# Kernel tuning notes

Measured on AMD Instinct MI355X. Metric: run time of the kernel, lower is better.

## Reference

```python
import jax, jax.numpy as jnp
import numpy as np

BATCH, INPUT_SIZE, HIDDEN = 128, 32, 1024


def setup_inputs() -> dict:
    key = jax.random.key(0)
    k1, k2, k3, k4 = jax.random.split(key, 4)
    idx = jax.random.randint(k1, (BATCH,), 0, INPUT_SIZE)
    inp = jax.nn.one_hot(idx, INPUT_SIZE, dtype=jnp.float32)  # one-hot per assert
    state = jax.random.normal(k2, (1, BATCH, HIDDEN), dtype=jnp.float32)
    weight = jax.random.normal(k3, (HIDDEN, HIDDEN, INPUT_SIZE), dtype=jnp.float32) * 0.02
    bias = jax.random.normal(k4, (HIDDEN, INPUT_SIZE), dtype=jnp.float32) * 0.02
    return {"input": inp, "state": state, "weight": weight, "bias": bias}


def reference(input, state, weight, bias):
    # Faithful to SRUCell.forward: one-hot selection of per-input weight/bias,
    # expressed as contractions (same math, no [B,H,H,I] materialization).
    hx = state[0]                                             # [B, H]
    # rec_temp = sum_j sum_i weight[h,j,i] * input[b,i] * hx[b,j]
    rec_temp = jnp.einsum('hji,bi,bj->bh', weight, input, hx)  # [B, H]
    trial_bias = jnp.einsum('hi,bi->bh', bias, input)          # [B, H]
    hy = hx + rec_temp + trial_bias
    return hy[None, ...]                                       # [1, B, H]
```

## Files before the change

kernel.cpp:

```cpp
#include <hip/hip_runtime.h>


constexpr int B  = 128;
constexpr int I  = 32;
constexpr int H  = 1024;
constexpr int K  = H * I;
constexpr int BM = 128;
constexpr int BK = 64;
constexpr int SPLIT = 32;
constexpr int KC = K / SPLIT;
constexpr int NT = KC / BK;

typedef short  short8 __attribute__((ext_vector_type(8)));
typedef float  f32x4  __attribute__((ext_vector_type(4)));

__device__ __forceinline__ unsigned short f2bf(float f) {
    unsigned u = __builtin_bit_cast(unsigned, f);
    return (unsigned short)((u + 0x7FFFu + ((u >> 16) & 1u)) >> 16);
}

__global__ void sru_idx_kernel(const float* __restrict__ inp,
                               int* __restrict__ idx, float* __restrict__ val) {
    int b = threadIdx.x;
    if (b >= B) return;
    float best = inp[b * I];
    int bi = 0;
#pragma unroll
    for (int i = 1; i < I; ++i) {
        float v = inp[b * I + i];
        if (v > best) { best = v; bi = i; }
    }
    idx[b] = bi;
    val[b] = best;
}

__global__ __launch_bounds__(256) void sru_init_kernel(
    const float* __restrict__ hx, const float* __restrict__ bias,
    const int* __restrict__ idx, const float* __restrict__ val,
    float* __restrict__ out) {
    int e = blockIdx.x * 256 + threadIdx.x;
    int b = e >> 10, h = e & (H - 1);
    out[e] = hx[e] + val[b] * bias[h * I + idx[b]];
}

__global__ __launch_bounds__(256) void sru_reduce_kernel(
    const float* __restrict__ hx, const float* __restrict__ bias,
    const int* __restrict__ idx, const float* __restrict__ val,
    const float* __restrict__ partial, float* __restrict__ out) {
    int e  = blockIdx.x * 256 + threadIdx.x;
    int b  = e >> 8;
    int h4 = (e & 255) * 4;
    float4 s = *reinterpret_cast<const float4*>(&hx[b * H + h4]);
    int ib = idx[b];
    float v = val[b];
    s.x += v * bias[(h4 + 0) * I + ib];
    s.y += v * bias[(h4 + 1) * I + ib];
    s.z += v * bias[(h4 + 2) * I + ib];
    s.w += v * bias[(h4 + 3) * I + ib];
#pragma unroll
    for (int sp = 0; sp < SPLIT; ++sp) {
        float4 p = *reinterpret_cast<const float4*>(
            &partial[((size_t)sp * B + b) * H + h4]);
        s.x += p.x; s.y += p.y; s.z += p.z; s.w += p.w;
    }
    *reinterpret_cast<float4*>(&out[b * H + h4]) = s;
}

template <bool USE_WS>
__global__ __launch_bounds__(512, 1) void sru_gemm_kernel(
    const float* __restrict__ hx, const float* __restrict__ w,
    const int* __restrict__ idx, const float* __restrict__ val,
    float* __restrict__ out) {
    __shared__ __align__(16) unsigned short As[BM * BK];
    __shared__ __align__(16) unsigned short Xs[B * BK];
    __shared__ __align__(16) unsigned short hxs[B * 32];

    const int tid = threadIdx.x;
    const int h0  = blockIdx.x * BM;
    const int kc0 = blockIdx.y * KC;

    {
        int b  = tid >> 2;
        int c0 = (tid & 3) * 8;
        const float* p = hx + b * H + blockIdx.y * 32 + c0;
        float4 v0 = *reinterpret_cast<const float4*>(p);
        float4 v1 = *reinterpret_cast<const float4*>(p + 4);
        float vb = val[b];
        short8 s;
        s[0] = (short)f2bf(v0.x * vb); s[1] = (short)f2bf(v0.y * vb);
        s[2] = (short)f2bf(v0.z * vb); s[3] = (short)f2bf(v0.w * vb);
        s[4] = (short)f2bf(v1.x * vb); s[5] = (short)f2bf(v1.y * vb);
        s[6] = (short)f2bf(v1.z * vb); s[7] = (short)f2bf(v1.w * vb);
        *reinterpret_cast<short8*>(&hxs[b * 32 + c0]) = s;
    }

    const int arow = tid >> 2;
    const int akq  = (tid & 3) * 16;
    const float* ap = w + (size_t)(h0 + arow) * K + kc0 + akq;
    const int ag0 = ((akq >> 3) + 0) ^ (arow & 7);
    const int ag1 = ((akq >> 3) + 1) ^ (arow & 7);

    const int xb  = arow;
    const int ib  = idx[xb];
    const int i0  = akq & 31;
    const int jadd = akq >> 5;
    const int xg0 = ag0, xg1 = ag1;

    const int lane = tid & 63;
    const int wid  = tid >> 6;
    const int wm = wid & 1;
    const int wn = wid >> 1;
    const int kg = lane >> 4;
    int aoff[4][2], boff[2][2];
#pragma unroll
    for (int fm = 0; fm < 4; ++fm) {
        int r = wm * 64 + fm * 16 + (lane & 15);
#pragma unroll
        for (int ks = 0; ks < 2; ++ks)
            aoff[fm][ks] = r * 64 + ((ks * 4 + kg) ^ (r & 7)) * 8;
    }
#pragma unroll
    for (int fn = 0; fn < 2; ++fn) {
        int r = wn * 32 + fn * 16 + (lane & 15);
#pragma unroll
        for (int ks = 0; ks < 2; ++ks)
            boff[fn][ks] = r * 64 + ((ks * 4 + kg) ^ (r & 7)) * 8;
    }

    f32x4 acc[4][2];
#pragma unroll
    for (int fm = 0; fm < 4; ++fm)
#pragma unroll
        for (int fn = 0; fn < 2; ++fn)
            acc[fm][fn] = f32x4{0.f, 0.f, 0.f, 0.f};

    auto writeA = [&](float4 a0, float4 a1, float4 a2, float4 a3) {
        short8 s0, s1;
        s0[0] = (short)f2bf(a0.x); s0[1] = (short)f2bf(a0.y);
        s0[2] = (short)f2bf(a0.z); s0[3] = (short)f2bf(a0.w);
        s0[4] = (short)f2bf(a1.x); s0[5] = (short)f2bf(a1.y);
        s0[6] = (short)f2bf(a1.z); s0[7] = (short)f2bf(a1.w);
        s1[0] = (short)f2bf(a2.x); s1[1] = (short)f2bf(a2.y);
        s1[2] = (short)f2bf(a2.z); s1[3] = (short)f2bf(a2.w);
        s1[4] = (short)f2bf(a3.x); s1[5] = (short)f2bf(a3.y);
        s1[6] = (short)f2bf(a3.z); s1[7] = (short)f2bf(a3.w);
        *reinterpret_cast<short8*>(&As[arow * 64 + ag0 * 8]) = s0;
        *reinterpret_cast<short8*>(&As[arow * 64 + ag1 * 8]) = s1;
    };
    auto writeX = [&](int t) {
        int jloc = t * 2 + jadd;
        short hv = (short)hxs[xb * 32 + jloc];
        short8 x0, x1;
#pragma unroll
        for (int e = 0; e < 8; ++e) {
            x0[e] = (i0 + e == ib) ? hv : (short)0;
            x1[e] = (i0 + 8 + e == ib) ? hv : (short)0;
        }
        *reinterpret_cast<short8*>(&Xs[xb * 64 + xg0 * 8]) = x0;
        *reinterpret_cast<short8*>(&Xs[xb * 64 + xg1 * 8]) = x1;
    };
    auto compute = [&]() {
#pragma unroll
        for (int ks = 0; ks < 2; ++ks) {
            short8 af[4], bfr[2];
#pragma unroll
            for (int fm = 0; fm < 4; ++fm)
                af[fm] = *reinterpret_cast<const short8*>(&As[aoff[fm][ks]]);
#pragma unroll
            for (int fn = 0; fn < 2; ++fn)
                bfr[fn] = *reinterpret_cast<const short8*>(&Xs[boff[fn][ks]]);
#pragma unroll
            for (int fm = 0; fm < 4; ++fm)
#pragma unroll
                for (int fn = 0; fn < 2; ++fn)
                    acc[fm][fn] = __builtin_amdgcn_mfma_f32_16x16x32_bf16(
                        af[fm], bfr[fn], acc[fm][fn], 0, 0, 0);
        }
    };

    float4 r0 = *reinterpret_cast<const float4*>(ap + 0);
    float4 r1 = *reinterpret_cast<const float4*>(ap + 4);
    float4 r2 = *reinterpret_cast<const float4*>(ap + 8);
    float4 r3 = *reinterpret_cast<const float4*>(ap + 12);
    __syncthreads();
    writeX(0);
    writeA(r0, r1, r2, r3);
    __syncthreads();

    for (int t = 0; t < NT; ++t) {
        if (t + 1 < NT) {
            const float* p = ap + (t + 1) * BK;
            r0 = *reinterpret_cast<const float4*>(p + 0);
            r1 = *reinterpret_cast<const float4*>(p + 4);
            r2 = *reinterpret_cast<const float4*>(p + 8);
            r3 = *reinterpret_cast<const float4*>(p + 12);
        }
        compute();
        __syncthreads();
        if (t + 1 < NT) {
            writeA(r0, r1, r2, r3);
            writeX(t + 1);
        }
        __syncthreads();
    }

    if constexpr (USE_WS) {
        float* pp = out + (size_t)blockIdx.y * B * H;
#pragma unroll
        for (int fm = 0; fm < 4; ++fm) {
#pragma unroll
            for (int fn = 0; fn < 2; ++fn) {
                int n  = wn * 32 + fn * 16 + (lane & 15);
                int m0 = wm * 64 + fm * 16 + (lane >> 4) * 4;
                float4 vv = {acc[fm][fn][0], acc[fm][fn][1],
                             acc[fm][fn][2], acc[fm][fn][3]};
                *reinterpret_cast<float4*>(&pp[(size_t)n * H + h0 + m0]) = vv;
            }
        }
    } else {
#pragma unroll
        for (int fm = 0; fm < 4; ++fm) {
#pragma unroll
            for (int fn = 0; fn < 2; ++fn) {
                int n  = wn * 32 + fn * 16 + (lane & 15);
                int m0 = wm * 64 + fm * 16 + (lane >> 4) * 4;
#pragma unroll
                for (int rr = 0; rr < 4; ++rr)
                    atomicAdd(&out[(size_t)n * H + h0 + m0 + rr], acc[fm][fn][rr]);
            }
        }
    }
}

extern "C" void kernel_launch(void* const* d_in, const int* in_sizes, int n_in,
                              void* d_out, int out_size, void* d_ws, size_t ws_size,
                              hipStream_t stream) {
    const float* inp    = (const float*)d_in[0];
    const float* state  = (const float*)d_in[1];
    const float* weight = (const float*)d_in[2];
    const float* bias   = (const float*)d_in[3];
    float* out = (float*)d_out;

    int*   idx = (int*)d_ws;
    float* val = (float*)((char*)d_ws + B * sizeof(int));
    float* partial = (float*)((char*)d_ws + 1024);
    const size_t need = 1024 + (size_t)SPLIT * B * H * sizeof(float);

    sru_idx_kernel<<<1, B, 0, stream>>>(inp, idx, val);

    if (ws_size >= need) {
        sru_gemm_kernel<true><<<dim3(H / BM, SPLIT), 512, 0, stream>>>(
            state, weight, idx, val, partial);
        sru_reduce_kernel<<<(B * H / 4) / 256, 256, 0, stream>>>(
            state, bias, idx, val, partial, out);
    } else {
        sru_init_kernel<<<(B * H) / 256, 256, 0, stream>>>(state, bias, idx, val, out);
        sru_gemm_kernel<false><<<dim3(H / BM, SPLIT), 512, 0, stream>>>(
            state, weight, idx, val, out);
    }
}
```

Measured before the change: 41.98 us.

## Fuse argmax into kernels, build one-hot X in registers, double-buffer smaller tiles

Removes the separate argmax kernel launch. Each GEMM and reduce block now recomputes the one-hot index itself. The shared-memory X tile is replaced by register masks applied to the scaled hidden value, so the X shared writes go away. BM is halved to 64, giving twice as many blocks, and the A tile is double-buffered in shared memory so one barrier per iteration is enough. Occupancy hints are raised. In exchange there is redundant argmax work per block and less reuse of each B fragment across M.

```diff
diff --git a/kernel.cpp b/kernel.cpp
--- a/kernel.cpp
+++ b/kernel.cpp
@@ -5,13 +5,14 @@
 constexpr int I  = 32;
 constexpr int H  = 1024;
 constexpr int K  = H * I;
-constexpr int BM = 128;
+constexpr int BM = 64;
 constexpr int BK = 64;
 constexpr int SPLIT = 32;
 constexpr int KC = K / SPLIT;
 constexpr int NT = KC / BK;
 
 typedef short  short8 __attribute__((ext_vector_type(8)));
+typedef unsigned int uint4v __attribute__((ext_vector_type(4)));
 typedef float  f32x4  __attribute__((ext_vector_type(4)));
 
 __device__ __forceinline__ unsigned short f2bf(float f) {
@@ -19,10 +20,8 @@
     return (unsigned short)((u + 0x7FFFu + ((u >> 16) & 1u)) >> 16);
 }
 
-__global__ void sru_idx_kernel(const float* __restrict__ inp,
-                               int* __restrict__ idx, float* __restrict__ val) {
-    int b = threadIdx.x;
-    if (b >= B) return;
+__device__ __forceinline__ void argmax32(const float* __restrict__ inp, int b,
+                                         int& ib, float& vb) {
     float best = inp[b * I];
     int bi = 0;
 #pragma unroll
@@ -30,29 +29,26 @@
         float v = inp[b * I + i];
         if (v > best) { best = v; bi = i; }
     }
-    idx[b] = bi;
-    val[b] = best;
+    ib = bi; vb = best;
 }
 
 __global__ __launch_bounds__(256) void sru_init_kernel(
-    const float* __restrict__ hx, const float* __restrict__ bias,
-    const int* __restrict__ idx, const float* __restrict__ val,
-    float* __restrict__ out) {
+    const float* __restrict__ inp, const float* __restrict__ hx,
+    const float* __restrict__ bias, float* __restrict__ out) {
     int e = blockIdx.x * 256 + threadIdx.x;
     int b = e >> 10, h = e & (H - 1);
-    out[e] = hx[e] + val[b] * bias[h * I + idx[b]];
+    int ib; float v; argmax32(inp, b, ib, v);
+    out[e] = hx[e] + v * bias[h * I + ib];
 }
 
 __global__ __launch_bounds__(256) void sru_reduce_kernel(
-    const float* __restrict__ hx, const float* __restrict__ bias,
-    const int* __restrict__ idx, const float* __restrict__ val,
-    const float* __restrict__ partial, float* __restrict__ out) {
-    int e  = blockIdx.x * 256 + threadIdx.x;
-    int b  = e >> 8;
-    int h4 = (e & 255) * 4;
+    const float* __restrict__ inp, const float* __restrict__ hx,
+    const float* __restrict__ bias, const float* __restrict__ partial,
+    float* __restrict__ out) {
+    const int b  = blockIdx.x;
+    const int h4 = threadIdx.x * 4;
+    int ib; float v; argmax32(inp, b, ib, v);
     float4 s = *reinterpret_cast<const float4*>(&hx[b * H + h4]);
-    int ib = idx[b];
-    float v = val[b];
     s.x += v * bias[(h4 + 0) * I + ib];
     s.y += v * bias[(h4 + 1) * I + ib];
     s.z += v * bias[(h4 + 2) * I + ib];
@@ -67,25 +63,32 @@
 }
 
 template <bool USE_WS>
-__global__ __launch_bounds__(512, 1) void sru_gemm_kernel(
-    const float* __restrict__ hx, const float* __restrict__ w,
-    const int* __restrict__ idx, const float* __restrict__ val,
-    float* __restrict__ out) {
-    __shared__ __align__(16) unsigned short As[BM * BK];
-    __shared__ __align__(16) unsigned short Xs[B * BK];
+__global__ __launch_bounds__(512, 4) void sru_gemm_kernel(
+    const float* __restrict__ inp, const float* __restrict__ hx,
+    const float* __restrict__ w, float* __restrict__ out) {
+    __shared__ __align__(16) unsigned short As[2][BM * BK];
     __shared__ __align__(16) unsigned short hxs[B * 32];
+    __shared__ int   idxs[B];
+    __shared__ float vals[B];
 
     const int tid = threadIdx.x;
     const int h0  = blockIdx.x * BM;
-    const int kc0 = blockIdx.y * KC;
+    const int by  = blockIdx.y;
+    const int kc0 = by * KC;
+
+    if (tid < B) {
+        int ib; float vb; argmax32(inp, tid, ib, vb);
+        idxs[tid] = ib; vals[tid] = vb;
+    }
+    __syncthreads();
 
     {
         int b  = tid >> 2;
         int c0 = (tid & 3) * 8;
-        const float* p = hx + b * H + blockIdx.y * 32 + c0;
+        const float* p = hx + b * H + by * 32 + c0;
         float4 v0 = *reinterpret_cast<const float4*>(p);
         float4 v1 = *reinterpret_cast<const float4*>(p + 4);
-        float vb = val[b];
+        float vb = vals[b];
         short8 s;
         s[0] = (short)f2bf(v0.x * vb); s[1] = (short)f2bf(v0.y * vb);
         s[2] = (short)f2bf(v0.z * vb); s[3] = (short)f2bf(v0.w * vb);
@@ -94,124 +97,113 @@
         *reinterpret_cast<short8*>(&hxs[b * 32 + c0]) = s;
     }
 
-    const int arow = tid >> 2;
-    const int akq  = (tid & 3) * 16;
-    const float* ap = w + (size_t)(h0 + arow) * K + kc0 + akq;
-    const int ag0 = ((akq >> 3) + 0) ^ (arow & 7);
-    const int ag1 = ((akq >> 3) + 1) ^ (arow & 7);
-
-    const int xb  = arow;
-    const int ib  = idx[xb];
-    const int i0  = akq & 31;
-    const int jadd = akq >> 5;
-    const int xg0 = ag0, xg1 = ag1;
+    const int arow = tid >> 3;
+    const int ag   = tid & 7;
+    const float* ap = w + (size_t)(h0 + arow) * K + kc0 + ag * 8;
+    const int awoff = arow * 64 + (ag ^ (arow & 7)) * 8;
+
+    float4 r0, r1;
+    auto loadA = [&](int t) {
+        const float* p = ap + t * BK;
+        r0 = *reinterpret_cast<const float4*>(p);
+        r1 = *reinterpret_cast<const float4*>(p + 4);
+    };
+    auto writeA = [&](int buf) {
+        short8 s;
+        s[0] = (short)f2bf(r0.x); s[1] = (short)f2bf(r0.y);
+        s[2] = (short)f2bf(r0.z); s[3] = (short)f2bf(r0.w);
+        s[4] = (short)f2bf(r1.x); s[5] = (short)f2bf(r1.y);
+        s[6] = (short)f2bf(r1.z); s[7] = (short)f2bf(r1.w);
+        *reinterpret_cast<short8*>(&As[buf][awoff]) = s;
+    };
 
     const int lane = tid & 63;
     const int wid  = tid >> 6;
     const int wm = wid & 1;
     const int wn = wid >> 1;
     const int kg = lane >> 4;
-    int aoff[4][2], boff[2][2];
-#pragma unroll
-    for (int fm = 0; fm < 4; ++fm) {
-        int r = wm * 64 + fm * 16 + (lane & 15);
+
+    int aoff[2][2];
+#pragma unroll
+    for (int fm = 0; fm < 2; ++fm) {
+        int r = wm * 32 + fm * 16 + (lane & 15);
 #pragma unroll
         for (int ks = 0; ks < 2; ++ks)
-            aoff[fm][ks] = r * 64 + ((ks * 4 + kg) ^ (r & 7)) * 8;
-    }
+            aoff[fm][ks] = r * 64 + (((ks * 4 + kg) ^ (r & 7))) * 8;
+    }
+
+    int bcol[2];
+    uint4v msk[2];
 #pragma unroll
     for (int fn = 0; fn < 2; ++fn) {
-        int r = wn * 32 + fn * 16 + (lane & 15);
-#pragma unroll
-        for (int ks = 0; ks < 2; ++ks)
-            boff[fn][ks] = r * 64 + ((ks * 4 + kg) ^ (r & 7)) * 8;
-    }
-
-    f32x4 acc[4][2];
-#pragma unroll
-    for (int fm = 0; fm < 4; ++fm)
+        bcol[fn] = wn * 32 + fn * 16 + (lane & 15);
+        int rel = idxs[bcol[fn]] - kg * 8;
+        uint4v m;
+#pragma unroll
+        for (int q = 0; q < 4; ++q) {
+            unsigned lo = (rel == 2 * q)     ? 0xFFFFu : 0u;
+            unsigned hi = (rel == 2 * q + 1) ? 0xFFFFu : 0u;
+            m[q] = lo | (hi << 16);
+        }
+        msk[fn] = m;
+    }
+
+    f32x4 acc[2][2];
+#pragma unroll
+    for (int fm = 0; fm < 2; ++fm)
 #pragma unroll
         for (int fn = 0; fn < 2; ++fn)
             acc[fm][fn] = f32x4{0.f, 0.f, 0.f, 0.f};
 
-    auto writeA = [&](float4 a0, float4 a1, float4 a2, float4 a3) {
-        short8 s0, s1;
-        s0[0] = (short)f2bf(a0.x); s0[1] = (short)f2bf(a0.y);
-        s0[2] = (short)f2bf(a0.z); s0[3] = (short)f2bf(a0.w);
-        s0[4] = (short)f2bf(a1.x); s0[5] = (short)f2bf(a1.y);
-        s0[6] = (short)f2bf(a1.z); s0[7] = (short)f2bf(a1.w);
-        s1[0] = (short)f2bf(a2.x); s1[1] = (short)f2bf(a2.y);
-        s1[2] = (short)f2bf(a2.z); s1[3] = (short)f2bf(a2.w);
-        s1[4] = (short)f2bf(a3.x); s1[5] = (short)f2bf(a3.y);
-        s1[6] = (short)f2bf(a3.z); s1[7] = (short)f2bf(a3.w);
-        *reinterpret_cast<short8*>(&As[arow * 64 + ag0 * 8]) = s0;
-        *reinterpret_cast<short8*>(&As[arow * 64 + ag1 * 8]) = s1;
-    };
-    auto writeX = [&](int t) {
-        int jloc = t * 2 + jadd;
-        short hv = (short)hxs[xb * 32 + jloc];
-        short8 x0, x1;
-#pragma unroll
-        for (int e = 0; e < 8; ++e) {
-            x0[e] = (i0 + e == ib) ? hv : (short)0;
-            x1[e] = (i0 + 8 + e == ib) ? hv : (short)0;
-        }
-        *reinterpret_cast<short8*>(&Xs[xb * 64 + xg0 * 8]) = x0;
-        *reinterpret_cast<short8*>(&Xs[xb * 64 + xg1 * 8]) = x1;
-    };
-    auto compute = [&]() {
+    auto compute = [&](int buf, int t) {
 #pragma unroll
         for (int ks = 0; ks < 2; ++ks) {
-            short8 af[4], bfr[2];
-#pragma unroll
-            for (int fm = 0; fm < 4; ++fm)
-                af[fm] = *reinterpret_cast<const short8*>(&As[aoff[fm][ks]]);
-#pragma unroll
-            for (int fn = 0; fn < 2; ++fn)
-                bfr[fn] = *reinterpret_cast<const short8*>(&Xs[boff[fn][ks]]);
-#pragma unroll
-            for (int fm = 0; fm < 4; ++fm)
+            short8 af[2], xf[2];
+#pragma unroll
+            for (int fm = 0; fm < 2; ++fm)
+                af[fm] = *reinterpret_cast<const short8*>(&As[buf][aoff[fm][ks]]);
+#pragma unroll
+            for (int fn = 0; fn < 2; ++fn) {
+                unsigned hv = hxs[bcol[fn] * 32 + t * 2 + ks];
+                unsigned hv32 = hv | (hv << 16);
+                uint4v xd;
+#pragma unroll
+                for (int q = 0; q < 4; ++q) xd[q] = msk[fn][q] & hv32;
+                xf[fn] = __builtin_bit_cast(short8, xd);
+            }
+#pragma unroll
+            for (int fm = 0; fm < 2; ++fm)
 #pragma unroll
                 for (int fn = 0; fn < 2; ++fn)
                     acc[fm][fn] = __builtin_amdgcn_mfma_f32_16x16x32_bf16(
-                        af[fm], bfr[fn], acc[fm][fn], 0, 0, 0);
+                        af[fm], xf[fn], acc[fm][fn], 0, 0, 0);
         }
     };
 
-    float4 r0 = *reinterpret_cast<const float4*>(ap + 0);
-    float4 r1 = *reinterpret_cast<const float4*>(ap + 4);
-    float4 r2 = *reinterpret_cast<const float4*>(ap + 8);
-    float4 r3 = *reinterpret_cast<const float4*>(ap + 12);
+    loadA(0);
     __syncthreads();
-    writeX(0);
-    writeA(r0, r1, r2, r3);
+    writeA(0);
+    loadA(1);
     __syncthreads();
-
+    int cur = 0;
     for (int t = 0; t < NT; ++t) {
         if (t + 1 < NT) {
-            const float* p = ap + (t + 1) * BK;
-            r0 = *reinterpret_cast<const float4*>(p + 0);
-            r1 = *reinterpret_cast<const float4*>(p + 4);
-            r2 = *reinterpret_cast<const float4*>(p + 8);
-            r3 = *reinterpret_cast<const float4*>(p + 12);
-        }
-        compute();
+            writeA(cur ^ 1);
+            if (t + 2 < NT) loadA(t + 2);
+        }
+        compute(cur, t);
         __syncthreads();
-        if (t + 1 < NT) {
-            writeA(r0, r1, r2, r3);
-            writeX(t + 1);
-        }
-        __syncthreads();
+        cur ^= 1;
     }
 
     if constexpr (USE_WS) {
-        float* pp = out + (size_t)blockIdx.y * B * H;
-#pragma unroll
-        for (int fm = 0; fm < 4; ++fm) {
+        float* pp = out + (size_t)by * (B * H);
+#pragma unroll
+        for (int fm = 0; fm < 2; ++fm) {
 #pragma unroll
             for (int fn = 0; fn < 2; ++fn) {
-                int n  = wn * 32 + fn * 16 + (lane & 15);
-                int m0 = wm * 64 + fm * 16 + (lane >> 4) * 4;
+                int n  = bcol[fn];
+                int m0 = wm * 32 + fm * 16 + (lane >> 4) * 4;
                 float4 vv = {acc[fm][fn][0], acc[fm][fn][1],
                              acc[fm][fn][2], acc[fm][fn][3]};
                 *reinterpret_cast<float4*>(&pp[(size_t)n * H + h0 + m0]) = vv;
@@ -219,11 +211,11 @@
         }
     } else {
 #pragma unroll
-        for (int fm = 0; fm < 4; ++fm) {
+        for (int fm = 0; fm < 2; ++fm) {
 #pragma unroll
             for (int fn = 0; fn < 2; ++fn) {
-                int n  = wn * 32 + fn * 16 + (lane & 15);
-                int m0 = wm * 64 + fm * 16 + (lane >> 4) * 4;
+                int n  = bcol[fn];
+                int m0 = wm * 32 + fm * 16 + (lane >> 4) * 4;
 #pragma unroll
                 for (int rr = 0; rr < 4; ++rr)
                     atomicAdd(&out[(size_t)n * H + h0 + m0 + rr], acc[fm][fn][rr]);
@@ -241,21 +233,17 @@
     const float* bias   = (const float*)d_in[3];
     float* out = (float*)d_out;
 
-    int*   idx = (int*)d_ws;
-    float* val = (float*)((char*)d_ws + B * sizeof(int));
-    float* partial = (float*)((char*)d_ws + 1024);
-    const size_t need = 1024 + (size_t)SPLIT * B * H * sizeof(float);
-
-    sru_idx_kernel<<<1, B, 0, stream>>>(inp, idx, val);
+    float* partial = (float*)d_ws;
+    const size_t need = (size_t)SPLIT * B * H * sizeof(float);
 
     if (ws_size >= need) {
         sru_gemm_kernel<true><<<dim3(H / BM, SPLIT), 512, 0, stream>>>(
-            state, weight, idx, val, partial);
-        sru_reduce_kernel<<<(B * H / 4) / 256, 256, 0, stream>>>(
-            state, bias, idx, val, partial, out);
+            inp, state, weight, partial);
+        sru_reduce_kernel<<<B, 256, 0, stream>>>(
+            inp, state, bias, partial, out);
     } else {
-        sru_init_kernel<<<(B * H) / 256, 256, 0, stream>>>(state, bias, idx, val, out);
+        sru_init_kernel<<<(B * H) / 256, 256, 0, stream>>>(inp, state, bias, out);
         sru_gemm_kernel<false><<<dim3(H / BM, SPLIT), 512, 0, stream>>>(
-            state, weight, idx, val, out);
-    }
-}
+            inp, state, weight, out);
+    }
+}
```

Result: faster. 35.28 us (-16.0%).
